# Kernel tuning notes

Hardware: AMD Instinct MI355X
Metric: run time of the kernel (lower is better)

The kernel has to match this reference:

```python
import jax, jax.numpy as jnp
import numpy as np

INF_SUB_NUM = -9000000000000000.0
LN_EPS = 1e-5


def _layernorm(x, gamma, beta):
    mu = jnp.mean(x, axis=-1, keepdims=True)
    var = jnp.mean(jnp.square(x - mu), axis=-1, keepdims=True)
    return gamma * (x - mu) * jax.lax.rsqrt(var + LN_EPS) + beta


def setup_inputs() -> dict:
    key = jax.random.key(0)
    kh, ke, kt, kw1, kw2 = jax.random.split(key, 5)
    B, N, E, D = 8, 4096, 2048, 256
    stdv = 1.0 / np.sqrt(D)
    return {
        "hidden": jax.random.normal(kh, (B, N, D), dtype=jnp.float32),
        "ht": jax.random.randint(kt, (B, E, N), 0, 2, dtype=jnp.int32),
        "edge_emb": jax.random.normal(ke, (B, E, D), dtype=jnp.float32),
        "wnk": jax.random.uniform(kw1, (D, D), jnp.float32, -stdv, stdv),
        "wek": jax.random.uniform(kw2, (D, D), jnp.float32, -stdv, stdv),
        "ln_gamma": jnp.ones((D,), jnp.float32),
        "ln_beta": jnp.zeros((D,), jnp.float32),
    }


def reference(hidden, ht, edge_emb, wnk, wek, ln_gamma, ln_beta):
    # hidden: [B,N,D]; ht: [B,E,N] incidence; edge_emb: [B,E,D]
    D = hidden.shape[-1]
    scale = 1.0 / jnp.sqrt(jnp.float32(D))

    edge_emb = _layernorm(edge_emb, ln_gamma, ln_beta)          # [B,E,D]
    node_k = hidden @ wnk                                        # [B,N,D]

    # Stage 1: edges attend over their incident nodes (softmax over N, dim=2)
    edge_scores = jnp.einsum('bed,bnd->ben', edge_emb, node_k) * scale
    edge_scores = jnp.where(ht > 0, edge_scores, INF_SUB_NUM)
    attn_edge = jax.nn.softmax(edge_scores, axis=2)              # [B,E,N]
    edge_h = jnp.einsum('ben,bnd->bed', attn_edge, hidden) + edge_emb

    # Stage 2: nodes gather from edges; softmax over N (dim=1), as in source
    edge_k = edge_h @ wek                                        # [B,E,D]
    node_scores = jnp.einsum('bnd,bed->bne', node_k, edge_k) * scale
    node_scores = jnp.where(jnp.transpose(ht, (0, 2, 1)) > 0, node_scores, INF_SUB_NUM)
    attn_node = jax.nn.softmax(node_scores, axis=1)              # [B,N,E]
    node_hidden = jnp.einsum('bne,bed->bnd', attn_node, edge_h)  # [B,N,D]
    return node_hidden
```

## Files before the change

kernel.cpp:

```cpp
#include <hip/hip_runtime.h>
#include <hip/hip_bf16.h>
#include <stdint.h>


#define B_ 8
#define N_ 4096
#define E_ 2048
#define D_ 256
#define INF_SUB (-9.0e15f)

typedef short bf16x8 __attribute__((ext_vector_type(8)));
typedef float f32x4 __attribute__((ext_vector_type(4)));
typedef unsigned short us8 __attribute__((ext_vector_type(8)));

#define AS1 __attribute__((address_space(1)))
#define AS3 __attribute__((address_space(3)))

__device__ __forceinline__ unsigned short f2bf(float f) {
    union { float f; unsigned int u; } v; v.f = f;
    unsigned int r = v.u + 0x7fffu + ((v.u >> 16) & 1u);
    return (unsigned short)(r >> 16);
}
__device__ __forceinline__ float bf2f(unsigned short h) {
    union { unsigned int u; float f; } v; v.u = ((unsigned int)h) << 16;
    return v.f;
}
__device__ __forceinline__ float waveReduceSum(float v) {
#pragma unroll
    for (int o = 32; o > 0; o >>= 1) v += __shfl_xor(v, o, 64);
    return v;
}

__global__ __launch_bounds__(256) void ln_kernel(const float* __restrict__ x,
                                                 const float* __restrict__ gamma,
                                                 const float* __restrict__ beta,
                                                 unsigned short* __restrict__ yb) {
    __shared__ float red[8];
    const int row = blockIdx.x;
    const int t = threadIdx.x;
    const int lane = t & 63, wid = t >> 6;
    const float v = x[(size_t)row * D_ + t];
    float s = waveReduceSum(v);
    if (lane == 0) red[wid] = s;
    __syncthreads();
    const float mu = (red[0] + red[1] + red[2] + red[3]) * (1.0f / D_);
    const float d = v - mu;
    float s2 = waveReduceSum(d * d);
    if (lane == 0) red[4 + wid] = s2;
    __syncthreads();
    const float var = (red[4] + red[5] + red[6] + red[7]) * (1.0f / D_);
    yb[(size_t)row * D_ + t] = f2bf(gamma[t] * d * rsqrtf(var + 1e-5f) + beta[t]);
}

__global__ __launch_bounds__(256) void pack_mask(const int* __restrict__ ht,
                                                 uint32_t* __restrict__ bits) {
    __shared__ __align__(8) unsigned char nib[256];
    const int row = blockIdx.x;
    const int t = threadIdx.x;
    const int* hrow = ht + (size_t)row * N_;
    uint32_t* brow = bits + (size_t)row * (N_ / 32);
#pragma unroll
    for (int it = 0; it < 4; ++it) {
        const int4 v = *(const int4*)&hrow[it * 1024 + t * 4];
        unsigned char n = (unsigned char)((v.x > 0) | ((v.y > 0) << 1) |
                                          ((v.z > 0) << 2) | ((v.w > 0) << 3));
        nib[t] = n;
        __syncthreads();
        if (t < 32) {
            uint64_t x = *(const uint64_t*)&nib[t * 8];
            x = (x | (x >> 4)) & 0x00FF00FF00FF00FFull;
            x = (x | (x >> 8)) & 0x0000FFFF0000FFFFull;
            brow[it * 32 + t] = (uint32_t)(x | (x >> 16));
        }
        __syncthreads();
    }
}

__global__ __launch_bounds__(256) void prep_hidden(const float* __restrict__ in,
                                                   unsigned short* __restrict__ hb,
                                                   unsigned short* __restrict__ hT) {
    __shared__ unsigned short tile[64][65];
    const int b = blockIdx.z;
    in += (size_t)b * N_ * D_;
    hb += (size_t)b * N_ * D_;
    hT += (size_t)b * D_ * N_;
    const int n0 = blockIdx.y * 64, d0 = blockIdx.x * 64;
    const int t = threadIdx.x;
    const int tr = t >> 4, tc = (t & 15) * 4;
#pragma unroll
    for (int q = 0; q < 4; ++q) {
        const int rr = q * 16 + tr;
        const float4 f = *(const float4*)&in[(size_t)(n0 + rr) * D_ + d0 + tc];
        unsigned short h0 = f2bf(f.x), h1 = f2bf(f.y), h2 = f2bf(f.z), h3 = f2bf(f.w);
        *(ushort4*)&hb[(size_t)(n0 + rr) * D_ + d0 + tc] = make_ushort4(h0, h1, h2, h3);
        tile[rr][tc + 0] = h0; tile[rr][tc + 1] = h1;
        tile[rr][tc + 2] = h2; tile[rr][tc + 3] = h3;
    }
    __syncthreads();
#pragma unroll
    for (int q = 0; q < 4; ++q) {
        const int cc = q * 16 + tr;
        ushort4 o = make_ushort4(tile[tc + 0][cc], tile[tc + 1][cc],
                                 tile[tc + 2][cc], tile[tc + 3][cc]);
        *(ushort4*)&hT[(size_t)(d0 + cc) * N_ + n0 + tc] = o;
    }
}

__global__ __launch_bounds__(256) void cast_wT(const float* __restrict__ w,
                                               unsigned short* __restrict__ wT) {
    const int gid = blockIdx.x * 256 + threadIdx.x;
    const int i = gid >> 8, j = gid & 255;
    wT[j * D_ + i] = f2bf(w[i * D_ + j]);
}

__global__ __launch_bounds__(256) void reduce_pv(const float* __restrict__ slab,
                                                 const unsigned short* __restrict__ eln,
                                                 const float* __restrict__ rsum,
                                                 unsigned short* __restrict__ eh,
                                                 float* __restrict__ ehT) {
    __shared__ float tile[64][65];
    const int b = blockIdx.z;
    const float* s0 = slab + (size_t)(b * 2) * E_ * D_;
    const float* s1 = slab + (size_t)(b * 2 + 1) * E_ * D_;
    const int e0 = blockIdx.y * 64, d0 = blockIdx.x * 64;
    const int t = threadIdx.x;
    const int tr = t >> 4, tc = (t & 15) * 4;
#pragma unroll
    for (int q = 0; q < 4; ++q) {
        const int rr = q * 16 + tr;
        const int row = e0 + rr;
        const float4 v0 = *(const float4*)&s0[(size_t)row * D_ + d0 + tc];
        const float4 v1 = *(const float4*)&s1[(size_t)row * D_ + d0 + tc];
        const float inv = 1.0f / rsum[(size_t)b * E_ + row];
        const ushort4 el = *(const ushort4*)&eln[(size_t)b * E_ * D_ + (size_t)row * D_ + d0 + tc];
        const float x0 = (v0.x + v1.x) * inv + bf2f(el.x);
        const float x1 = (v0.y + v1.y) * inv + bf2f(el.y);
        const float x2 = (v0.z + v1.z) * inv + bf2f(el.z);
        const float x3 = (v0.w + v1.w) * inv + bf2f(el.w);
        *(ushort4*)&eh[(size_t)b * E_ * D_ + (size_t)row * D_ + d0 + tc] =
            make_ushort4(f2bf(x0), f2bf(x1), f2bf(x2), f2bf(x3));
        tile[rr][tc + 0] = x0; tile[rr][tc + 1] = x1;
        tile[rr][tc + 2] = x2; tile[rr][tc + 3] = x3;
    }
    __syncthreads();
#pragma unroll
    for (int q = 0; q < 4; ++q) {
        const int cc = q * 16 + tr;
        float4 o = make_float4(tile[tc + 0][cc], tile[tc + 1][cc],
                               tile[tc + 2][cc], tile[tc + 3][cc]);
        *(float4*)&ehT[(size_t)b * D_ * E_ + (size_t)(d0 + cc) * E_ + e0 + tc] = o;
    }
}

__global__ __launch_bounds__(256) void scale_ehT(const float* __restrict__ ehT,
                                                 const float* __restrict__ lsum,
                                                 unsigned short* __restrict__ ehs) {
    const size_t base = ((size_t)blockIdx.x * 256 + threadIdx.x) * 8;
    const int b = (int)(base / ((size_t)D_ * E_));
    const int e = (int)(base % E_);
    const float4 f0 = *(const float4*)&ehT[base];
    const float4 f1 = *(const float4*)&ehT[base + 4];
    const float4 l0 = *(const float4*)&lsum[(size_t)b * E_ + e];
    const float4 l1 = *(const float4*)&lsum[(size_t)b * E_ + e + 4];
    us8 o;
    o[0] = f2bf(f0.x / l0.x); o[1] = f2bf(f0.y / l0.y);
    o[2] = f2bf(f0.z / l0.z); o[3] = f2bf(f0.w / l0.w);
    o[4] = f2bf(f1.x / l1.x); o[5] = f2bf(f1.y / l1.y);
    o[6] = f2bf(f1.z / l1.z); o[7] = f2bf(f1.w / l1.w);
    *(us8*)&ehs[base] = o;
}

#define M_BF16 0
#define M_MASK 1
#define M_F32 2

template <int MODE, int MASKOR, int RSUM, int SPLIT, int CSUM, int SWZ>
__global__ __launch_bounds__(256) void mfma_gemm_nt(
        const short* __restrict__ A, const short* __restrict__ Bm,
        void* __restrict__ Cv, const uint32_t* __restrict__ bits,
        float* __restrict__ sums,
        int K, int ldc, size_t sA, size_t sB, size_t sC, float scale) {
    __shared__ __align__(16) short ls[(MODE == M_F32) ? 16384 : 16896];
    __shared__ uint32_t mwords[MASKOR ? 512 : 4];
    short* lsA = ls;
    short* lsB = ls + 8192;
    int bx = blockIdx.x, by = blockIdx.y, bz = blockIdx.z;
    if (SWZ) {
        const int gx = gridDim.x, gy = gridDim.y;
        int lin = bx + gx * (by + gy * bz);
        const int nwg = gx * gy * (int)gridDim.z;
        lin = (lin & 7) * (nwg >> 3) + (lin >> 3);
        bx = lin % gx;
        const int t2 = lin / gx;
        by = t2 % gy;
        bz = t2 / gy;
    }
    const int zb = bz;
    const int b = SPLIT ? (zb >> 1) : zb;
    A += (size_t)b * sA;
    Bm += (size_t)b * sB;
    const int m0 = by * 128, n0 = bx * 128;
    const int tid = threadIdx.x, wid = tid >> 6, lane = tid & 63;
    const int l15 = lane & 15, kg = lane >> 4;
    const int wr = wid >> 1, wc = wid & 1;

    if (MASKOR) {
        const uint32_t* bb = bits + (size_t)b * E_ * (N_ / 32);
#pragma unroll
        for (int q = 0; q < 2; ++q) {
            const int idx = q * 256 + tid;
            mwords[idx] = (MASKOR == 1)
                ? bb[(size_t)(m0 + (idx >> 2)) * (N_ / 32) + (n0 >> 5) + (idx & 3)]
                : bb[(size_t)(n0 + (idx >> 2)) * (N_ / 32) + (m0 >> 5) + (idx & 3)];
        }
    }

    int raoff[4], rota[4], rboff[4], rotb[4];
#pragma unroll
    for (int i = 0; i < 4; ++i) {
        const int ra = wr * 64 + i * 16 + l15;
        raoff[i] = ra * 64; rota[i] = kg + (ra >> 1);
        const int rb = wc * 64 + i * 16 + l15;
        rboff[i] = rb * 64; rotb[i] = kg + (rb >> 1);
    }
    const f32x4 zero = {0.f, 0.f, 0.f, 0.f};
    f32x4 acc[4][4];
#pragma unroll
    for (int i = 0; i < 4; ++i)
#pragma unroll
        for (int j = 0; j < 4; ++j) acc[i][j] = zero;

    const int kt0 = SPLIT ? (zb & 1) * (K >> 1) : 0;
    const int ktE = SPLIT ? kt0 + (K >> 1) : K;
    for (int kt = kt0; kt < ktE; kt += 64) {
        __syncthreads();
#pragma unroll
        for (int q = 0; q < 4; ++q) {
            const int c = q * 256 + tid;
            const int r = c >> 3;
            const int kc = ((c & 7) - (r >> 1)) & 7;
            const short* ga = A + (size_t)(m0 + r) * K + kt + kc * 8;
            __builtin_amdgcn_global_load_lds((const AS1 void*)ga,
                (AS3 void*)(lsA + (q * 256 + wid * 64) * 8), 16, 0, 0);
            const short* gb = Bm + (size_t)(n0 + r) * K + kt + kc * 8;
            __builtin_amdgcn_global_load_lds((const AS1 void*)gb,
                (AS3 void*)(lsB + (q * 256 + wid * 64) * 8), 16, 0, 0);
        }
        __syncthreads();
#pragma unroll
        for (int s = 0; s < 2; ++s) {
            bf16x8 fa[4], fb[4];
#pragma unroll
            for (int i = 0; i < 4; ++i)
                fa[i] = *(const bf16x8*)(lsA + raoff[i] + (((s * 4 + rota[i]) & 7) << 3));
#pragma unroll
            for (int j = 0; j < 4; ++j)
                fb[j] = *(const bf16x8*)(lsB + rboff[j] + (((s * 4 + rotb[j]) & 7) << 3));
#pragma unroll
            for (int i = 0; i < 4; ++i)
#pragma unroll
                for (int j = 0; j < 4; ++j)
                    acc[i][j] = __builtin_amdgcn_mfma_f32_16x16x32_bf16(fa[i], fb[j], acc[i][j], 0, 0, 0);
        }
    }

    __syncthreads();

    if (MODE == M_F32) {
        float* C = (float*)Cv + (SPLIT ? (size_t)zb * sC : (size_t)b * sC);
        float* lsF = (float*)ls;
#pragma unroll
        for (int h = 0; h < 4; ++h) {
            if (wr == (h >> 1)) {
#pragma unroll
                for (int ii = 0; ii < 2; ++ii) {
                    const int i = (h & 1) * 2 + ii;
#pragma unroll
                    for (int j = 0; j < 4; ++j)
#pragma unroll
                        for (int r = 0; r < 4; ++r) {
                            const int rl = ii * 16 + kg * 4 + r;
                            const int cl = wc * 64 + j * 16 + l15;
                            lsF[rl * 128 + cl] = acc[i][j][r];
                        }
                }
            }
            __syncthreads();
#pragma unroll
            for (int si = 0; si < 4; ++si) {
                const int row = (tid >> 5) + si * 8;
                const int colb = (tid & 31) * 4;
                float4 v = *(float4*)&lsF[row * 128 + colb];
                *(float4*)&C[(size_t)(m0 + h * 32 + row) * ldc + n0 + colb] = v;
            }
            __syncthreads();
        }
    } else {
        unsigned short* C = (unsigned short*)Cv + (size_t)b * sC;
        float evsum[4] = {0.f, 0.f, 0.f, 0.f};
#pragma unroll
        for (int i = 0; i < 4; ++i) {
#pragma unroll
            for (int r = 0; r < 4; ++r) {
                const int rowfull = wr * 64 + i * 16 + kg * 4 + r;
                uint64_t mwr = 0;
                if (MODE == M_MASK && MASKOR == 1)
                    mwr = *(const uint64_t*)&mwords[rowfull * 4 + wc * 2];
                float rs = 0.f;
#pragma unroll
                for (int j = 0; j < 4; ++j) {
                    const int cl = wc * 64 + j * 16 + l15;
                    float v = acc[i][j][r];
                    if (MODE == M_MASK) {
                        v *= scale;
                        uint32_t bit;
                        if (MASKOR == 1) {
                            bit = (uint32_t)(mwr >> (j * 16 + l15)) & 1u;
                        } else {
                            const uint64_t mwc = *(const uint64_t*)&mwords[cl * 4 + wr * 2];
                            bit = (uint32_t)(mwc >> (i * 16 + kg * 4 + r)) & 1u;
                        }
                        v = bit ? __expf(v) : 0.f;
                        if (CSUM) evsum[j] += v;
                        if (RSUM) rs += v;
                    }
                    ls[rowfull * 132 + cl] = (short)f2bf(v);
                }
                if (RSUM) {
                    rs += __shfl_xor(rs, 1, 64);
                    rs += __shfl_xor(rs, 2, 64);
                    rs += __shfl_xor(rs, 4, 64);
                    rs += __shfl_xor(rs, 8, 64);
                    if (l15 == 0)
                        atomicAdd(&sums[(size_t)b * E_ + m0 + rowfull], rs);
                }
            }
        }
        __syncthreads();
#pragma unroll
        for (int si = 0; si < 8; ++si) {
            const int row = (tid >> 4) + si * 16;
            const int col = (tid & 15) * 8;
            us8 val = *(us8*)&ls[row * 132 + col];
            *(us8*)&C[(size_t)(m0 + row) * ldc + n0 + col] = val;
        }
        if (CSUM) {
#pragma unroll
            for (int j = 0; j < 4; ++j) {
                float cs = evsum[j];
                cs += __shfl_xor(cs, 16, 64);
                cs += __shfl_xor(cs, 32, 64);
                if (kg == 0)
                    atomicAdd(&sums[(size_t)b * E_ + n0 + wc * 64 + j * 16 + l15], cs);
            }
        }
    }
}

extern "C" void kernel_launch(void* const* d_in, const int* in_sizes, int n_in,
                              void* d_out, int out_size, void* d_ws, size_t ws_size,
                              hipStream_t stream) {
    const float* hidden = (const float*)d_in[0];
    const int* ht = (const int*)d_in[1];
    const float* edge_emb = (const float*)d_in[2];
    const float* wnk = (const float*)d_in[3];
    const float* wek = (const float*)d_in[4];
    const float* gamma = (const float*)d_in[5];
    const float* beta = (const float*)d_in[6];
    float* out = (float*)d_out;
    (void)in_sizes; (void)n_in; (void)out_size; (void)ws_size;

    char* w = (char*)d_ws;
    unsigned short* SP = (unsigned short*)w;         w += (size_t)B_ * E_ * N_ * 2;
    unsigned short* hidden_bf = (unsigned short*)w;  w += (size_t)B_ * N_ * D_ * 2;
    unsigned short* hiddenT_bf = (unsigned short*)w; w += (size_t)B_ * D_ * N_ * 2;
    unsigned short* node_k_bf = (unsigned short*)w;  w += (size_t)B_ * N_ * D_ * 2;
    unsigned short* eln_bf = (unsigned short*)w;     w += (size_t)B_ * E_ * D_ * 2;
    unsigned short* edge_h_bf = (unsigned short*)w;  w += (size_t)B_ * E_ * D_ * 2;
    float* ehT_f32 = (float*)w;                      w += (size_t)B_ * D_ * E_ * 4;
    unsigned short* ehsT_bf = (unsigned short*)w;    w += (size_t)B_ * D_ * E_ * 2;
    unsigned short* edge_k_bf = (unsigned short*)w;  w += (size_t)B_ * E_ * D_ * 2;
    float* slabs = (float*)w;                        w += (size_t)B_ * 2 * E_ * D_ * 4;
    uint32_t* bits = (uint32_t*)w;                   w += (size_t)B_ * E_ * (N_ / 32) * 4;
    float* rsum = (float*)w;                         w += (size_t)B_ * E_ * 4;
    float* lsum = (float*)w;                         w += (size_t)B_ * E_ * 4;
    unsigned short* wnkT = (unsigned short*)w;       w += (size_t)D_ * D_ * 2;
    unsigned short* wekT = (unsigned short*)w;       w += (size_t)D_ * D_ * 2;

    const float scale = 0.0625f;

    prep_hidden<<<dim3(D_ / 64, N_ / 64, B_), 256, 0, stream>>>(hidden, hidden_bf, hiddenT_bf);
    cast_wT<<<D_ * D_ / 256, 256, 0, stream>>>(wnk, wnkT);
    cast_wT<<<D_ * D_ / 256, 256, 0, stream>>>(wek, wekT);
    ln_kernel<<<B_ * E_, 256, 0, stream>>>(edge_emb, gamma, beta, eln_bf);
    pack_mask<<<B_ * E_, 256, 0, stream>>>(ht, bits);
    hipMemsetAsync(rsum, 0, (size_t)B_ * E_ * 8, stream);

    mfma_gemm_nt<M_BF16, 0, 0, 0, 0, 0><<<dim3(D_ / 128, (B_ * N_) / 128, 1), 256, 0, stream>>>(
        (const short*)hidden_bf, (const short*)wnkT, node_k_bf, nullptr, nullptr,
        D_, D_, 0, 0, 0, 1.f);
    mfma_gemm_nt<M_MASK, 1, 1, 0, 0, 1><<<dim3(N_ / 128, E_ / 128, B_), 256, 0, stream>>>(
        (const short*)eln_bf, (const short*)node_k_bf, SP, bits, rsum,
        D_, N_, (size_t)E_ * D_, (size_t)N_ * D_, (size_t)E_ * N_, scale);
    mfma_gemm_nt<M_F32, 0, 0, 1, 0, 1><<<dim3(D_ / 128, E_ / 128, B_ * 2), 256, 0, stream>>>(
        (const short*)SP, (const short*)hiddenT_bf, slabs, nullptr, nullptr,
        N_, D_, (size_t)E_ * N_, (size_t)D_ * N_, (size_t)E_ * D_, 1.f);
    reduce_pv<<<dim3(D_ / 64, E_ / 64, B_), 256, 0, stream>>>(
        slabs, eln_bf, rsum, edge_h_bf, ehT_f32);
    mfma_gemm_nt<M_BF16, 0, 0, 0, 0, 0><<<dim3(D_ / 128, (B_ * E_) / 128, 1), 256, 0, stream>>>(
        (const short*)edge_h_bf, (const short*)wekT, edge_k_bf, nullptr, nullptr,
        D_, D_, 0, 0, 0, 1.f);
    mfma_gemm_nt<M_MASK, 2, 0, 0, 1, 1><<<dim3(E_ / 128, N_ / 128, B_), 256, 0, stream>>>(
        (const short*)node_k_bf, (const short*)edge_k_bf, SP, bits, lsum,
        D_, E_, (size_t)N_ * D_, (size_t)E_ * D_, (size_t)N_ * E_, scale);
    scale_ehT<<<(B_ * D_ * E_) / (256 * 8), 256, 0, stream>>>(ehT_f32, lsum, ehsT_bf);
    mfma_gemm_nt<M_F32, 0, 0, 0, 0, 1><<<dim3(D_ / 128, N_ / 128, B_), 256, 0, stream>>>(
        (const short*)SP, (const short*)ehsT_bf, out, nullptr, nullptr,
        E_, D_, (size_t)N_ * E_, (size_t)D_ * E_, (size_t)N_ * D_, 1.f);
}
```

Measured before the change: 790.3 us.

## Add 64x256 wide GEMM for PV products, drop split-K slabs

Replaces the two attention-times-value GEMMs (K=4096 split-K into two fp32 slabs, and K=2048 output GEMM) with a new kernel using 64x256 output tiles spanning the full D dimension. The big probability matrix SP is then read once per row block instead of twice (once per 128-column D half), and the split-K slab reduction in reduce_pv goes away. The XCD-style block swizzle is removed from the generic GEMM and applied only in the wide kernel. The trade-off is less parallelism without split-K (256 blocks for stage 1) and more registers per thread (32 accumulators of 4 floats), which may lower occupancy.

```diff
diff --git a/kernel.cpp b/kernel.cpp
--- a/kernel.cpp
+++ b/kernel.cpp
@@ -120,8 +120,7 @@
                                                  float* __restrict__ ehT) {
     __shared__ float tile[64][65];
     const int b = blockIdx.z;
-    const float* s0 = slab + (size_t)(b * 2) * E_ * D_;
-    const float* s1 = slab + (size_t)(b * 2 + 1) * E_ * D_;
+    const float* s0 = slab + (size_t)b * E_ * D_;
     const int e0 = blockIdx.y * 64, d0 = blockIdx.x * 64;
     const int t = threadIdx.x;
     const int tr = t >> 4, tc = (t & 15) * 4;
@@ -130,13 +129,12 @@
         const int rr = q * 16 + tr;
         const int row = e0 + rr;
         const float4 v0 = *(const float4*)&s0[(size_t)row * D_ + d0 + tc];
-        const float4 v1 = *(const float4*)&s1[(size_t)row * D_ + d0 + tc];
         const float inv = 1.0f / rsum[(size_t)b * E_ + row];
         const ushort4 el = *(const ushort4*)&eln[(size_t)b * E_ * D_ + (size_t)row * D_ + d0 + tc];
-        const float x0 = (v0.x + v1.x) * inv + bf2f(el.x);
-        const float x1 = (v0.y + v1.y) * inv + bf2f(el.y);
-        const float x2 = (v0.z + v1.z) * inv + bf2f(el.z);
-        const float x3 = (v0.w + v1.w) * inv + bf2f(el.w);
+        const float x0 = v0.x * inv + bf2f(el.x);
+        const float x1 = v0.y * inv + bf2f(el.y);
+        const float x2 = v0.z * inv + bf2f(el.z);
+        const float x3 = v0.w * inv + bf2f(el.w);
         *(ushort4*)&eh[(size_t)b * E_ * D_ + (size_t)row * D_ + d0 + tc] =
             make_ushort4(f2bf(x0), f2bf(x1), f2bf(x2), f2bf(x3));
         tile[rr][tc + 0] = x0; tile[rr][tc + 1] = x1;
@@ -174,7 +172,7 @@
 #define M_MASK 1
 #define M_F32 2
 
-template <int MODE, int MASKOR, int RSUM, int SPLIT, int CSUM, int SWZ>
+template <int MODE, int MASKOR, int RSUM, int SPLIT, int CSUM>
 __global__ __launch_bounds__(256) void mfma_gemm_nt(
         const short* __restrict__ A, const short* __restrict__ Bm,
         void* __restrict__ Cv, const uint32_t* __restrict__ bits,
@@ -184,22 +182,11 @@
     __shared__ uint32_t mwords[MASKOR ? 512 : 4];
     short* lsA = ls;
     short* lsB = ls + 8192;
-    int bx = blockIdx.x, by = blockIdx.y, bz = blockIdx.z;
-    if (SWZ) {
-        const int gx = gridDim.x, gy = gridDim.y;
-        int lin = bx + gx * (by + gy * bz);
-        const int nwg = gx * gy * (int)gridDim.z;
-        lin = (lin & 7) * (nwg >> 3) + (lin >> 3);
-        bx = lin % gx;
-        const int t2 = lin / gx;
-        by = t2 % gy;
-        bz = t2 / gy;
-    }
-    const int zb = bz;
+    const int zb = blockIdx.z;
     const int b = SPLIT ? (zb >> 1) : zb;
     A += (size_t)b * sA;
     Bm += (size_t)b * sB;
-    const int m0 = by * 128, n0 = bx * 128;
+    const int m0 = blockIdx.y * 128, n0 = blockIdx.x * 128;
     const int tid = threadIdx.x, wid = tid >> 6, lane = tid & 63;
     const int l15 = lane & 15, kg = lane >> 4;
     const int wr = wid >> 1, wc = wid & 1;
@@ -357,6 +344,110 @@
     }
 }
 
+__global__ __launch_bounds__(256) void mfma_gemm_wide(
+        const short* __restrict__ A, const short* __restrict__ Bm,
+        float* __restrict__ C,
+        int K, size_t sA, size_t sB, size_t sC) {
+    __shared__ __align__(16) short ls[20480];
+    short* lsA = ls;
+    short* lsB = ls + 4096;
+    const int gx = gridDim.x;
+    int lin = blockIdx.x + gx * blockIdx.y;
+    const int nwg = gx * (int)gridDim.y;
+    lin = (lin & 7) * (nwg >> 3) + (lin >> 3);
+    const int bm = lin % gx, bb = lin / gx;
+    A += (size_t)bb * sA;
+    Bm += (size_t)bb * sB;
+    C += (size_t)bb * sC;
+    const int m0 = bm * 64;
+    const int tid = threadIdx.x, wid = tid >> 6, lane = tid & 63;
+    const int l15 = lane & 15, kg = lane >> 4;
+    const int wr = wid >> 1, wc = wid & 1;
+
+    int raoff[2], rota[2], rboff[8], rotb[8];
+#pragma unroll
+    for (int i = 0; i < 2; ++i) {
+        const int ra = wr * 32 + i * 16 + l15;
+        raoff[i] = ra * 64; rota[i] = kg + (ra >> 1);
+    }
+#pragma unroll
+    for (int j = 0; j < 8; ++j) {
+        const int rb = wc * 128 + j * 16 + l15;
+        rboff[j] = rb * 64; rotb[j] = kg + (rb >> 1);
+    }
+    const f32x4 zero = {0.f, 0.f, 0.f, 0.f};
+    f32x4 acc[2][8];
+#pragma unroll
+    for (int i = 0; i < 2; ++i)
+#pragma unroll
+        for (int j = 0; j < 8; ++j) acc[i][j] = zero;
+
+    for (int kt = 0; kt < K; kt += 64) {
+        __syncthreads();
+#pragma unroll
+        for (int q = 0; q < 2; ++q) {
+            const int c = q * 256 + tid;
+            const int r = c >> 3;
+            const int kc = ((c & 7) - (r >> 1)) & 7;
+            const short* ga = A + (size_t)(m0 + r) * K + kt + kc * 8;
+            __builtin_amdgcn_global_load_lds((const AS1 void*)ga,
+                (AS3 void*)(lsA + (q * 256 + wid * 64) * 8), 16, 0, 0);
+        }
+#pragma unroll
+        for (int q = 0; q < 8; ++q) {
+            const int c = q * 256 + tid;
+            const int r = c >> 3;
+            const int kc = ((c & 7) - (r >> 1)) & 7;
+            const short* gb = Bm + (size_t)r * K + kt + kc * 8;
+            __builtin_amdgcn_global_load_lds((const AS1 void*)gb,
+                (AS3 void*)(lsB + (q * 256 + wid * 64) * 8), 16, 0, 0);
+        }
+        __syncthreads();
+#pragma unroll
+        for (int s = 0; s < 2; ++s) {
+            bf16x8 fa[2], fb[8];
+#pragma unroll
+            for (int i = 0; i < 2; ++i)
+                fa[i] = *(const bf16x8*)(lsA + raoff[i] + (((s * 4 + rota[i]) & 7) << 3));
+#pragma unroll
+            for (int j = 0; j < 8; ++j)
+                fb[j] = *(const bf16x8*)(lsB + rboff[j] + (((s * 4 + rotb[j]) & 7) << 3));
+#pragma unroll
+            for (int i = 0; i < 2; ++i)
+#pragma unroll
+                for (int j = 0; j < 8; ++j)
+                    acc[i][j] = __builtin_amdgcn_mfma_f32_16x16x32_bf16(fa[i], fb[j], acc[i][j], 0, 0, 0);
+        }
+    }
+
+    __syncthreads();
+    float* lsF = (float*)ls;
+#pragma unroll
+    for (int h = 0; h < 2; ++h) {
+        if (wr == h) {
+#pragma unroll
+            for (int i = 0; i < 2; ++i)
+#pragma unroll
+                for (int j = 0; j < 8; ++j)
+#pragma unroll
+                    for (int r = 0; r < 4; ++r) {
+                        const int row = i * 16 + kg * 4 + r;
+                        const int col = wc * 128 + j * 16 + l15;
+                        lsF[row * 256 + col] = acc[i][j][r];
+                    }
+        }
+        __syncthreads();
+#pragma unroll
+        for (int k = 0; k < 8; ++k) {
+            const int c = k * 256 + tid;
+            const int row = c >> 6;
+            const int c4 = (c & 63) * 4;
+            *(float4*)&C[(size_t)(m0 + h * 32 + row) * D_ + c4] = *(float4*)&lsF[row * 256 + c4];
+        }
+        __syncthreads();
+    }
+}
+
 extern "C" void kernel_launch(void* const* d_in, const int* in_sizes, int n_in,
                               void* d_out, int out_size, void* d_ws, size_t ws_size,
                               hipStream_t stream) {
@@ -380,7 +471,7 @@
     float* ehT_f32 = (float*)w;                      w += (size_t)B_ * D_ * E_ * 4;
     unsigned short* ehsT_bf = (unsigned short*)w;    w += (size_t)B_ * D_ * E_ * 2;
     unsigned short* edge_k_bf = (unsigned short*)w;  w += (size_t)B_ * E_ * D_ * 2;
-    float* slabs = (float*)w;                        w += (size_t)B_ * 2 * E_ * D_ * 4;
+    float* edge_sum = (float*)w;                     w += (size_t)B_ * E_ * D_ * 4;
     uint32_t* bits = (uint32_t*)w;                   w += (size_t)B_ * E_ * (N_ / 32) * 4;
     float* rsum = (float*)w;                         w += (size_t)B_ * E_ * 4;
     float* lsum = (float*)w;                         w += (size_t)B_ * E_ * 4;
@@ -396,25 +487,25 @@
     pack_mask<<<B_ * E_, 256, 0, stream>>>(ht, bits);
     hipMemsetAsync(rsum, 0, (size_t)B_ * E_ * 8, stream);
 
-    mfma_gemm_nt<M_BF16, 0, 0, 0, 0, 0><<<dim3(D_ / 128, (B_ * N_) / 128, 1), 256, 0, stream>>>(
+    mfma_gemm_nt<M_BF16, 0, 0, 0, 0><<<dim3(D_ / 128, (B_ * N_) / 128, 1), 256, 0, stream>>>(
         (const short*)hidden_bf, (const short*)wnkT, node_k_bf, nullptr, nullptr,
         D_, D_, 0, 0, 0, 1.f);
-    mfma_gemm_nt<M_MASK, 1, 1, 0, 0, 1><<<dim3(N_ / 128, E_ / 128, B_), 256, 0, stream>>>(
+    mfma_gemm_nt<M_MASK, 1, 1, 0, 0><<<dim3(N_ / 128, E_ / 128, B_), 256, 0, stream>>>(
         (const short*)eln_bf, (const short*)node_k_bf, SP, bits, rsum,
         D_, N_, (size_t)E_ * D_, (size_t)N_ * D_, (size_t)E_ * N_, scale);
-    mfma_gemm_nt<M_F32, 0, 0, 1, 0, 1><<<dim3(D_ / 128, E_ / 128, B_ * 2), 256, 0, stream>>>(
-        (const short*)SP, (const short*)hiddenT_bf, slabs, nullptr, nullptr,
-        N_, D_, (size_t)E_ * N_, (size_t)D_ * N_, (size_t)E_ * D_, 1.f);
+    mfma_gemm_wide<<<dim3(E_ / 64, B_), 256, 0, stream>>>(
+        (const short*)SP, (const short*)hiddenT_bf, edge_sum,
+        N_, (size_t)E_ * N_, (size_t)D_ * N_, (size_t)E_ * D_);
     reduce_pv<<<dim3(D_ / 64, E_ / 64, B_), 256, 0, stream>>>(
-        slabs, eln_bf, rsum, edge_h_bf, ehT_f32);
-    mfma_gemm_nt<M_BF16, 0, 0, 0, 0, 0><<<dim3(D_ / 128, (B_ * E_) / 128, 1), 256, 0, stream>>>(
+        edge_sum, eln_bf, rsum, edge_h_bf, ehT_f32);
+    mfma_gemm_nt<M_BF16, 0, 0, 0, 0><<<dim3(D_ / 128, (B_ * E_) / 128, 1), 256, 0, stream>>>(
         (const short*)edge_h_bf, (const short*)wekT, edge_k_bf, nullptr, nullptr,
         D_, D_, 0, 0, 0, 1.f);
-    mfma_gemm_nt<M_MASK, 2, 0, 0, 1, 1><<<dim3(E_ / 128, N_ / 128, B_), 256, 0, stream>>>(
+    mfma_gemm_nt<M_MASK, 2, 0, 0, 1><<<dim3(E_ / 128, N_ / 128, B_), 256, 0, stream>>>(
         (const short*)node_k_bf, (const short*)edge_k_bf, SP, bits, lsum,
         D_, E_, (size_t)N_ * D_, (size_t)E_ * D_, (size_t)N_ * E_, scale);
     scale_ehT<<<(B_ * D_ * E_) / (256 * 8), 256, 0, stream>>>(ehT_f32, lsum, ehsT_bf);
-    mfma_gemm_nt<M_F32, 0, 0, 0, 0, 1><<<dim3(D_ / 128, N_ / 128, B_), 256, 0, stream>>>(
-        (const short*)SP, (const short*)ehsT_bf, out, nullptr, nullptr,
-        E_, D_, (size_t)N_ * E_, (size_t)D_ * E_, (size_t)N_ * D_, 1.f);
-}
+    mfma_gemm_wide<<<dim3(N_ / 64, B_), 256, 0, stream>>>(
+        (const short*)SP, (const short*)ehsT_bf, out,
+        E_, (size_t)N_ * E_, (size_t)D_ * E_, (size_t)N_ * D_);
+}
```

Result: no change. 802.9 us (+1.6%).

## Fuse masked score, exp and PV GEMMs into flash-style attention kernels

Applied to the files above, without the earlier changes.

Replaces the separate score-GEMM, materialized bf16 probability matrix SP, and PV GEMM with fused kernels that compute masked exp scores per 64-column tile, stage them through LDS, and immediately accumulate P·V in registers. This removes the large B×E×N intermediate round-trip through global memory, the split-K slabs, the reduce kernel, and atomics. For stage 2 the column sums are computed in a separate score-only pass (MODE 0), and the scores are recomputed in the final fused pass, so that GEMM is done twice. It also uses large LDS and one block per CU, which may limit occupancy.

```diff
diff --git a/kernel.cpp b/kernel.cpp
--- a/kernel.cpp
+++ b/kernel.cpp
@@ -7,7 +7,6 @@
 #define N_ 4096
 #define E_ 2048
 #define D_ 256
-#define INF_SUB (-9.0e15f)
 
 typedef short bf16x8 __attribute__((ext_vector_type(8)));
 typedef float f32x4 __attribute__((ext_vector_type(4)));
@@ -113,45 +112,6 @@
     wT[j * D_ + i] = f2bf(w[i * D_ + j]);
 }
 
-__global__ __launch_bounds__(256) void reduce_pv(const float* __restrict__ slab,
-                                                 const unsigned short* __restrict__ eln,
-                                                 const float* __restrict__ rsum,
-                                                 unsigned short* __restrict__ eh,
-                                                 float* __restrict__ ehT) {
-    __shared__ float tile[64][65];
-    const int b = blockIdx.z;
-    const float* s0 = slab + (size_t)(b * 2) * E_ * D_;
-    const float* s1 = slab + (size_t)(b * 2 + 1) * E_ * D_;
-    const int e0 = blockIdx.y * 64, d0 = blockIdx.x * 64;
-    const int t = threadIdx.x;
-    const int tr = t >> 4, tc = (t & 15) * 4;
-#pragma unroll
-    for (int q = 0; q < 4; ++q) {
-        const int rr = q * 16 + tr;
-        const int row = e0 + rr;
-        const float4 v0 = *(const float4*)&s0[(size_t)row * D_ + d0 + tc];
-        const float4 v1 = *(const float4*)&s1[(size_t)row * D_ + d0 + tc];
-        const float inv = 1.0f / rsum[(size_t)b * E_ + row];
-        const ushort4 el = *(const ushort4*)&eln[(size_t)b * E_ * D_ + (size_t)row * D_ + d0 + tc];
-        const float x0 = (v0.x + v1.x) * inv + bf2f(el.x);
-        const float x1 = (v0.y + v1.y) * inv + bf2f(el.y);
-        const float x2 = (v0.z + v1.z) * inv + bf2f(el.z);
-        const float x3 = (v0.w + v1.w) * inv + bf2f(el.w);
-        *(ushort4*)&eh[(size_t)b * E_ * D_ + (size_t)row * D_ + d0 + tc] =
-            make_ushort4(f2bf(x0), f2bf(x1), f2bf(x2), f2bf(x3));
-        tile[rr][tc + 0] = x0; tile[rr][tc + 1] = x1;
-        tile[rr][tc + 2] = x2; tile[rr][tc + 3] = x3;
-    }
-    __syncthreads();
-#pragma unroll
-    for (int q = 0; q < 4; ++q) {
-        const int cc = q * 16 + tr;
-        float4 o = make_float4(tile[tc + 0][cc], tile[tc + 1][cc],
-                               tile[tc + 2][cc], tile[tc + 3][cc]);
-        *(float4*)&ehT[(size_t)b * D_ * E_ + (size_t)(d0 + cc) * E_ + e0 + tc] = o;
-    }
-}
-
 __global__ __launch_bounds__(256) void scale_ehT(const float* __restrict__ ehT,
                                                  const float* __restrict__ lsum,
                                                  unsigned short* __restrict__ ehs) {
@@ -170,50 +130,16 @@
     *(us8*)&ehs[base] = o;
 }
 
-#define M_BF16 0
-#define M_MASK 1
-#define M_F32 2
-
-template <int MODE, int MASKOR, int RSUM, int SPLIT, int CSUM, int SWZ>
-__global__ __launch_bounds__(256) void mfma_gemm_nt(
-        const short* __restrict__ A, const short* __restrict__ Bm,
-        void* __restrict__ Cv, const uint32_t* __restrict__ bits,
-        float* __restrict__ sums,
-        int K, int ldc, size_t sA, size_t sB, size_t sC, float scale) {
-    __shared__ __align__(16) short ls[(MODE == M_F32) ? 16384 : 16896];
-    __shared__ uint32_t mwords[MASKOR ? 512 : 4];
+__global__ __launch_bounds__(256) void gemm_bf16(const short* __restrict__ A,
+                                                 const short* __restrict__ Bm,
+                                                 unsigned short* __restrict__ C) {
+    __shared__ __align__(16) short ls[16896];
     short* lsA = ls;
     short* lsB = ls + 8192;
-    int bx = blockIdx.x, by = blockIdx.y, bz = blockIdx.z;
-    if (SWZ) {
-        const int gx = gridDim.x, gy = gridDim.y;
-        int lin = bx + gx * (by + gy * bz);
-        const int nwg = gx * gy * (int)gridDim.z;
-        lin = (lin & 7) * (nwg >> 3) + (lin >> 3);
-        bx = lin % gx;
-        const int t2 = lin / gx;
-        by = t2 % gy;
-        bz = t2 / gy;
-    }
-    const int zb = bz;
-    const int b = SPLIT ? (zb >> 1) : zb;
-    A += (size_t)b * sA;
-    Bm += (size_t)b * sB;
-    const int m0 = by * 128, n0 = bx * 128;
+    const int m0 = blockIdx.y * 128, n0 = blockIdx.x * 128;
     const int tid = threadIdx.x, wid = tid >> 6, lane = tid & 63;
     const int l15 = lane & 15, kg = lane >> 4;
     const int wr = wid >> 1, wc = wid & 1;
-
-    if (MASKOR) {
-        const uint32_t* bb = bits + (size_t)b * E_ * (N_ / 32);
-#pragma unroll
-        for (int q = 0; q < 2; ++q) {
-            const int idx = q * 256 + tid;
-            mwords[idx] = (MASKOR == 1)
-                ? bb[(size_t)(m0 + (idx >> 2)) * (N_ / 32) + (n0 >> 5) + (idx & 3)]
-                : bb[(size_t)(n0 + (idx >> 2)) * (N_ / 32) + (m0 >> 5) + (idx & 3)];
-        }
-    }
 
     int raoff[4], rota[4], rboff[4], rotb[4];
 #pragma unroll
@@ -230,19 +156,17 @@
 #pragma unroll
         for (int j = 0; j < 4; ++j) acc[i][j] = zero;
 
-    const int kt0 = SPLIT ? (zb & 1) * (K >> 1) : 0;
-    const int ktE = SPLIT ? kt0 + (K >> 1) : K;
-    for (int kt = kt0; kt < ktE; kt += 64) {
+    for (int kt = 0; kt < 256; kt += 64) {
         __syncthreads();
 #pragma unroll
         for (int q = 0; q < 4; ++q) {
             const int c = q * 256 + tid;
             const int r = c >> 3;
             const int kc = ((c & 7) - (r >> 1)) & 7;
-            const short* ga = A + (size_t)(m0 + r) * K + kt + kc * 8;
+            const short* ga = A + (size_t)(m0 + r) * 256 + kt + kc * 8;
             __builtin_amdgcn_global_load_lds((const AS1 void*)ga,
                 (AS3 void*)(lsA + (q * 256 + wid * 64) * 8), 16, 0, 0);
-            const short* gb = Bm + (size_t)(n0 + r) * K + kt + kc * 8;
+            const short* gb = Bm + (size_t)(n0 + r) * 256 + kt + kc * 8;
             __builtin_amdgcn_global_load_lds((const AS1 void*)gb,
                 (AS3 void*)(lsB + (q * 256 + wid * 64) * 8), 16, 0, 0);
         }
@@ -263,96 +187,268 @@
                     acc[i][j] = __builtin_amdgcn_mfma_f32_16x16x32_bf16(fa[i], fb[j], acc[i][j], 0, 0, 0);
         }
     }
-
     __syncthreads();
-
-    if (MODE == M_F32) {
-        float* C = (float*)Cv + (SPLIT ? (size_t)zb * sC : (size_t)b * sC);
+#pragma unroll
+    for (int i = 0; i < 4; ++i)
+#pragma unroll
+        for (int r = 0; r < 4; ++r) {
+            const int rowfull = wr * 64 + i * 16 + kg * 4 + r;
+#pragma unroll
+            for (int j = 0; j < 4; ++j) {
+                const int cl = wc * 64 + j * 16 + l15;
+                ls[rowfull * 132 + cl] = (short)f2bf(acc[i][j][r]);
+            }
+        }
+    __syncthreads();
+#pragma unroll
+    for (int si = 0; si < 8; ++si) {
+        const int row = (tid >> 4) + si * 16;
+        const int col = (tid & 15) * 8;
+        us8 val = *(us8*)&ls[row * 132 + col];
+        *(us8*)&C[(size_t)(m0 + row) * D_ + n0 + col] = val;
+    }
+}
+
+template <int MODE>
+__global__ __launch_bounds__(256, 1) void fused_attn(
+        const short* __restrict__ A, const short* __restrict__ B1,
+        const short* __restrict__ B2, const uint32_t* __restrict__ bits,
+        const unsigned short* __restrict__ eln,
+        void* __restrict__ out1, float* __restrict__ out2,
+        int KN, float scale) {
+    __shared__ __align__(16) short ls[(MODE == 0) ? 33024 : 69888];
+    const int b = blockIdx.x;
+    const int m0 = blockIdx.y * 64;
+    const int MA = (MODE == 2) ? N_ : E_;
+    const short* Ab = A + (size_t)b * MA * D_;
+    const short* B1b = B1 + (size_t)b * KN * D_;
+    const short* B2b = (MODE != 0) ? (B2 + (size_t)b * D_ * KN) : nullptr;
+    const uint32_t* bb = bits + (size_t)b * E_ * (N_ / 32);
+
+    const int tid = threadIdx.x, wid = tid >> 6, lane = tid & 63;
+    const int l15 = lane & 15, kg = lane >> 4;
+    const int wv = wid >> 1, ww = wid & 1;
+
+    bf16x8 fa[2][8];
+#pragma unroll
+    for (int mf = 0; mf < 2; ++mf) {
+        const size_t ar = (size_t)(m0 + wv * 32 + mf * 16 + l15) * D_;
+#pragma unroll
+        for (int kf = 0; kf < 8; ++kf)
+            fa[mf][kf] = *(const bf16x8*)(Ab + ar + (kf * 4 + kg) * 8);
+    }
+
+    const f32x4 zero = {0.f, 0.f, 0.f, 0.f};
+    f32x4 acco[2][8];
+    if (MODE != 0) {
+#pragma unroll
+        for (int mf = 0; mf < 2; ++mf)
+#pragma unroll
+            for (int jf = 0; jf < 8; ++jf) acco[mf][jf] = zero;
+    }
+    float rs[2][4] = {{0.f, 0.f, 0.f, 0.f}, {0.f, 0.f, 0.f, 0.f}};
+
+    short* Pp = ls + 65536;
+    const int NT = KN / 64;
+
+#define STAGE_T(db, tt) do {                                                   \
+        const int kt_ = (tt) * 64;                                             \
+        short* b1d_ = ls + (db) * 16384;                                       \
+        _Pragma("unroll")                                                      \
+        for (int q = 0; q < 8; ++q) {                                          \
+            const int c_ = q * 256 + tid;                                      \
+            const int r_ = c_ >> 5;                                            \
+            const int ck_ = (c_ & 31) ^ (r_ & 31);                             \
+            __builtin_amdgcn_global_load_lds(                                  \
+                (const AS1 void*)(B1b + (size_t)(kt_ + r_) * D_ + ck_ * 8),    \
+                (AS3 void*)(b1d_ + (q * 256 + wid * 64) * 8), 16, 0, 0);       \
+        }                                                                      \
+        if (MODE != 0) {                                                       \
+            short* b2d_ = ls + 32768 + (db) * 16384;                           \
+            _Pragma("unroll")                                                  \
+            for (int q = 0; q < 8; ++q) {                                      \
+                const int c_ = q * 256 + tid;                                  \
+                const int r_ = c_ >> 3;                                        \
+                const int ck_ = (c_ & 7) ^ ((r_ >> 1) & 7);                    \
+                __builtin_amdgcn_global_load_lds(                              \
+                    (const AS1 void*)(B2b + (size_t)r_ * KN + kt_ + ck_ * 8),  \
+                    (AS3 void*)(b2d_ + (q * 256 + wid * 64) * 8), 16, 0, 0);   \
+            }                                                                  \
+        }                                                                      \
+    } while (0)
+
+    STAGE_T(0, 0);
+    __syncthreads();
+
+    int cur = 0;
+    for (int t = 0; t < NT; ++t) {
+        if (t + 1 < NT) STAGE_T(cur ^ 1, t + 1);
+        const short* b1c = ls + cur * 16384;
+        f32x4 accs[2][2];
+        accs[0][0] = zero; accs[0][1] = zero; accs[1][0] = zero; accs[1][1] = zero;
+        const int rb0 = ww * 32 + l15, rb1 = ww * 32 + 16 + l15;
+        const int x0 = kg ^ (rb0 & 31), x1 = kg ^ (rb1 & 31);
+#pragma unroll
+        for (int kf = 0; kf < 8; ++kf) {
+            const bf16x8 fb0 = *(const bf16x8*)(b1c + rb0 * 256 + ((kf * 4) ^ x0) * 8);
+            const bf16x8 fb1 = *(const bf16x8*)(b1c + rb1 * 256 + ((kf * 4) ^ x1) * 8);
+            accs[0][0] = __builtin_amdgcn_mfma_f32_16x16x32_bf16(fa[0][kf], fb0, accs[0][0], 0, 0, 0);
+            accs[1][0] = __builtin_amdgcn_mfma_f32_16x16x32_bf16(fa[1][kf], fb0, accs[1][0], 0, 0, 0);
+            accs[0][1] = __builtin_amdgcn_mfma_f32_16x16x32_bf16(fa[0][kf], fb1, accs[0][1], 0, 0, 0);
+            accs[1][1] = __builtin_amdgcn_mfma_f32_16x16x32_bf16(fa[1][kf], fb1, accs[1][1], 0, 0, 0);
+        }
+        const int kt0 = t * 64;
+        uint64_t mw[2][4];
+        uint32_t cw[2];
+        if (MODE <= 1) {
+#pragma unroll
+            for (int mf = 0; mf < 2; ++mf)
+#pragma unroll
+                for (int r = 0; r < 4; ++r) {
+                    const int row = m0 + wv * 32 + mf * 16 + kg * 4 + r;
+                    mw[mf][r] = *(const uint64_t*)&bb[(size_t)row * (N_ / 32) + (kt0 >> 5)];
+                }
+        } else {
+#pragma unroll
+            for (int jf = 0; jf < 2; ++jf) {
+                const int col = kt0 + ww * 32 + jf * 16 + l15;
+                cw[jf] = bb[(size_t)col * (N_ / 32) + ((m0 + wv * 32) >> 5)];
+            }
+        }
+#pragma unroll
+        for (int mf = 0; mf < 2; ++mf)
+#pragma unroll
+            for (int jf = 0; jf < 2; ++jf)
+#pragma unroll
+                for (int r = 0; r < 4; ++r) {
+                    float v = accs[mf][jf][r] * scale;
+                    uint32_t bit;
+                    if (MODE <= 1)
+                        bit = (uint32_t)(mw[mf][r] >> (ww * 32 + jf * 16 + l15)) & 1u;
+                    else
+                        bit = (cw[jf] >> (mf * 16 + kg * 4 + r)) & 1u;
+                    v = bit ? __expf(v) : 0.f;
+                    if (MODE <= 1) rs[mf][r] += v;
+                    if (MODE != 0) {
+                        const int prow = wv * 32 + mf * 16 + kg * 4 + r;
+                        const int pcol = ww * 32 + jf * 16 + l15;
+                        Pp[prow * 64 + (((pcol >> 3) ^ ((prow >> 1) & 7)) * 8) + (pcol & 7)] =
+                            (short)f2bf(v);
+                    }
+                }
+        if (MODE != 0) {
+            __syncthreads();
+            const short* b2c = ls + 32768 + cur * 16384;
+            const int pr0 = wv * 32 + l15, pr1 = wv * 32 + 16 + l15;
+            const int px0 = kg ^ ((pr0 >> 1) & 7), px1 = kg ^ ((pr1 >> 1) & 7);
+#pragma unroll
+            for (int kf2 = 0; kf2 < 2; ++kf2) {
+                const bf16x8 pa0 = *(const bf16x8*)(Pp + pr0 * 64 + ((kf2 * 4) ^ px0) * 8);
+                const bf16x8 pa1 = *(const bf16x8*)(Pp + pr1 * 64 + ((kf2 * 4) ^ px1) * 8);
+#pragma unroll
+                for (int jf = 0; jf < 8; ++jf) {
+                    const int rh = ww * 128 + jf * 16 + l15;
+                    const bf16x8 fbh = *(const bf16x8*)(b2c + rh * 64 +
+                        (((kf2 * 4 + kg) ^ ((rh >> 1) & 7))) * 8);
+                    acco[0][jf] = __builtin_amdgcn_mfma_f32_16x16x32_bf16(pa0, fbh, acco[0][jf], 0, 0, 0);
+                    acco[1][jf] = __builtin_amdgcn_mfma_f32_16x16x32_bf16(pa1, fbh, acco[1][jf], 0, 0, 0);
+                }
+            }
+        }
+        __syncthreads();
+        cur ^= 1;
+    }
+#undef STAGE_T
+
+    if (MODE == 0) {
+        float* rsx = (float*)(ls + 32768);
+#pragma unroll
+        for (int mf = 0; mf < 2; ++mf)
+#pragma unroll
+            for (int r = 0; r < 4; ++r) {
+                float s = rs[mf][r];
+                s += __shfl_xor(s, 1, 64); s += __shfl_xor(s, 2, 64);
+                s += __shfl_xor(s, 4, 64); s += __shfl_xor(s, 8, 64);
+                if (l15 == 0) rsx[ww * 64 + wv * 32 + mf * 16 + kg * 4 + r] = s;
+            }
+        __syncthreads();
+        if (tid < 64)
+            ((float*)out1)[(size_t)b * E_ + m0 + tid] = rsx[tid] + rsx[64 + tid];
+    } else if (MODE == 1) {
+        float* rsx = (float*)(ls + 69632);
+#pragma unroll
+        for (int mf = 0; mf < 2; ++mf)
+#pragma unroll
+            for (int r = 0; r < 4; ++r) {
+                float s = rs[mf][r];
+                s += __shfl_xor(s, 1, 64); s += __shfl_xor(s, 2, 64);
+                s += __shfl_xor(s, 4, 64); s += __shfl_xor(s, 8, 64);
+                if (l15 == 0) rsx[ww * 64 + wv * 32 + mf * 16 + kg * 4 + r] = s;
+            }
+        __syncthreads();
         float* lsF = (float*)ls;
 #pragma unroll
-        for (int h = 0; h < 4; ++h) {
-            if (wr == (h >> 1)) {
-#pragma unroll
-                for (int ii = 0; ii < 2; ++ii) {
-                    const int i = (h & 1) * 2 + ii;
-#pragma unroll
-                    for (int j = 0; j < 4; ++j)
-#pragma unroll
-                        for (int r = 0; r < 4; ++r) {
-                            const int rl = ii * 16 + kg * 4 + r;
-                            const int cl = wc * 64 + j * 16 + l15;
-                            lsF[rl * 128 + cl] = acc[i][j][r];
-                        }
-                }
-            }
-            __syncthreads();
-#pragma unroll
-            for (int si = 0; si < 4; ++si) {
-                const int row = (tid >> 5) + si * 8;
-                const int colb = (tid & 31) * 4;
-                float4 v = *(float4*)&lsF[row * 128 + colb];
-                *(float4*)&C[(size_t)(m0 + h * 32 + row) * ldc + n0 + colb] = v;
-            }
-            __syncthreads();
+        for (int mf = 0; mf < 2; ++mf)
+#pragma unroll
+            for (int r = 0; r < 4; ++r) {
+                const int row = wv * 32 + mf * 16 + kg * 4 + r;
+                const float inv = 1.0f / (rsx[row] + rsx[64 + row]);
+#pragma unroll
+                for (int jf = 0; jf < 8; ++jf)
+                    lsF[row * 261 + ww * 128 + jf * 16 + l15] = acco[mf][jf][r] * inv;
+            }
+        __syncthreads();
+        unsigned short* ehb = (unsigned short*)out1 + (size_t)b * E_ * D_;
+        const unsigned short* elnb = eln + (size_t)b * E_ * D_;
+#pragma unroll
+        for (int p = 0; p < 8; ++p) {
+            const int idx = p * 2048 + tid * 8;
+            const int row = idx >> 8, col = idx & 255;
+            const us8 ev = *(const us8*)&elnb[(size_t)(m0 + row) * D_ + col];
+            us8 o;
+            float vv[8];
+#pragma unroll
+            for (int u = 0; u < 8; ++u) {
+                vv[u] = lsF[row * 261 + col + u] + bf2f(ev[u]);
+                o[u] = f2bf(vv[u]);
+            }
+            *(us8*)&ehb[(size_t)(m0 + row) * D_ + col] = o;
+#pragma unroll
+            for (int u = 0; u < 8; ++u)
+                lsF[row * 261 + col + u] = vv[u];
+        }
+        __syncthreads();
+        float* ehT = out2 + (size_t)b * D_ * E_;
+#pragma unroll
+        for (int p = 0; p < 8; ++p) {
+            const int idx = p * 2048 + tid * 8;
+            const int d = idx >> 6, e8 = idx & 63;
+            float4 v0, v1;
+            v0.x = lsF[(e8 + 0) * 261 + d]; v0.y = lsF[(e8 + 1) * 261 + d];
+            v0.z = lsF[(e8 + 2) * 261 + d]; v0.w = lsF[(e8 + 3) * 261 + d];
+            v1.x = lsF[(e8 + 4) * 261 + d]; v1.y = lsF[(e8 + 5) * 261 + d];
+            v1.z = lsF[(e8 + 6) * 261 + d]; v1.w = lsF[(e8 + 7) * 261 + d];
+            *(float4*)&ehT[(size_t)d * E_ + m0 + e8] = v0;
+            *(float4*)&ehT[(size_t)d * E_ + m0 + e8 + 4] = v1;
         }
     } else {
-        unsigned short* C = (unsigned short*)Cv + (size_t)b * sC;
-        float evsum[4] = {0.f, 0.f, 0.f, 0.f};
-#pragma unroll
-        for (int i = 0; i < 4; ++i) {
+        float* lsF = (float*)ls;
+#pragma unroll
+        for (int mf = 0; mf < 2; ++mf)
 #pragma unroll
             for (int r = 0; r < 4; ++r) {
-                const int rowfull = wr * 64 + i * 16 + kg * 4 + r;
-                uint64_t mwr = 0;
-                if (MODE == M_MASK && MASKOR == 1)
-                    mwr = *(const uint64_t*)&mwords[rowfull * 4 + wc * 2];
-                float rs = 0.f;
-#pragma unroll
-                for (int j = 0; j < 4; ++j) {
-                    const int cl = wc * 64 + j * 16 + l15;
-                    float v = acc[i][j][r];
-                    if (MODE == M_MASK) {
-                        v *= scale;
-                        uint32_t bit;
-                        if (MASKOR == 1) {
-                            bit = (uint32_t)(mwr >> (j * 16 + l15)) & 1u;
-                        } else {
-                            const uint64_t mwc = *(const uint64_t*)&mwords[cl * 4 + wr * 2];
-                            bit = (uint32_t)(mwc >> (i * 16 + kg * 4 + r)) & 1u;
-                        }
-                        v = bit ? __expf(v) : 0.f;
-                        if (CSUM) evsum[j] += v;
-                        if (RSUM) rs += v;
-                    }
-                    ls[rowfull * 132 + cl] = (short)f2bf(v);
-                }
-                if (RSUM) {
-                    rs += __shfl_xor(rs, 1, 64);
-                    rs += __shfl_xor(rs, 2, 64);
-                    rs += __shfl_xor(rs, 4, 64);
-                    rs += __shfl_xor(rs, 8, 64);
-                    if (l15 == 0)
-                        atomicAdd(&sums[(size_t)b * E_ + m0 + rowfull], rs);
-                }
-            }
-        }
-        __syncthreads();
-#pragma unroll
-        for (int si = 0; si < 8; ++si) {
-            const int row = (tid >> 4) + si * 16;
-            const int col = (tid & 15) * 8;
-            us8 val = *(us8*)&ls[row * 132 + col];
-            *(us8*)&C[(size_t)(m0 + row) * ldc + n0 + col] = val;
-        }
-        if (CSUM) {
-#pragma unroll
-            for (int j = 0; j < 4; ++j) {
-                float cs = evsum[j];
-                cs += __shfl_xor(cs, 16, 64);
-                cs += __shfl_xor(cs, 32, 64);
-                if (kg == 0)
-                    atomicAdd(&sums[(size_t)b * E_ + n0 + wc * 64 + j * 16 + l15], cs);
-            }
+                const int row = wv * 32 + mf * 16 + kg * 4 + r;
+#pragma unroll
+                for (int jf = 0; jf < 8; ++jf)
+                    lsF[row * 256 + ww * 128 + jf * 16 + l15] = acco[mf][jf][r];
+            }
+        __syncthreads();
+        float* ob = (float*)out1 + (size_t)b * N_ * D_;
+#pragma unroll
+        for (int p = 0; p < 16; ++p) {
+            const int lin = p * 256 + tid;
+            const int row = lin >> 6, c4 = (lin & 63) * 4;
+            *(float4*)&ob[(size_t)(m0 + row) * D_ + c4] = *(const float4*)&lsF[row * 256 + c4];
         }
     }
 }
@@ -371,7 +467,6 @@
     (void)in_sizes; (void)n_in; (void)out_size; (void)ws_size;
 
     char* w = (char*)d_ws;
-    unsigned short* SP = (unsigned short*)w;         w += (size_t)B_ * E_ * N_ * 2;
     unsigned short* hidden_bf = (unsigned short*)w;  w += (size_t)B_ * N_ * D_ * 2;
     unsigned short* hiddenT_bf = (unsigned short*)w; w += (size_t)B_ * D_ * N_ * 2;
     unsigned short* node_k_bf = (unsigned short*)w;  w += (size_t)B_ * N_ * D_ * 2;
@@ -380,9 +475,7 @@
     float* ehT_f32 = (float*)w;                      w += (size_t)B_ * D_ * E_ * 4;
     unsigned short* ehsT_bf = (unsigned short*)w;    w += (size_t)B_ * D_ * E_ * 2;
     unsigned short* edge_k_bf = (unsigned short*)w;  w += (size_t)B_ * E_ * D_ * 2;
-    float* slabs = (float*)w;                        w += (size_t)B_ * 2 * E_ * D_ * 4;
     uint32_t* bits = (uint32_t*)w;                   w += (size_t)B_ * E_ * (N_ / 32) * 4;
-    float* rsum = (float*)w;                         w += (size_t)B_ * E_ * 4;
     float* lsum = (float*)w;                         w += (size_t)B_ * E_ * 4;
     unsigned short* wnkT = (unsigned short*)w;       w += (size_t)D_ * D_ * 2;
     unsigned short* wekT = (unsigned short*)w;       w += (size_t)D_ * D_ * 2;
@@ -394,27 +487,19 @@
     cast_wT<<<D_ * D_ / 256, 256, 0, stream>>>(wek, wekT);
     ln_kernel<<<B_ * E_, 256, 0, stream>>>(edge_emb, gamma, beta, eln_bf);
     pack_mask<<<B_ * E_, 256, 0, stream>>>(ht, bits);
-    hipMemsetAsync(rsum, 0, (size_t)B_ * E_ * 8, stream);
-
-    mfma_gemm_nt<M_BF16, 0, 0, 0, 0, 0><<<dim3(D_ / 128, (B_ * N_) / 128, 1), 256, 0, stream>>>(
-        (const short*)hidden_bf, (const short*)wnkT, node_k_bf, nullptr, nullptr,
-        D_, D_, 0, 0, 0, 1.f);
-    mfma_gemm_nt<M_MASK, 1, 1, 0, 0, 1><<<dim3(N_ / 128, E_ / 128, B_), 256, 0, stream>>>(
-        (const short*)eln_bf, (const short*)node_k_bf, SP, bits, rsum,
-        D_, N_, (size_t)E_ * D_, (size_t)N_ * D_, (size_t)E_ * N_, scale);
-    mfma_gemm_nt<M_F32, 0, 0, 1, 0, 1><<<dim3(D_ / 128, E_ / 128, B_ * 2), 256, 0, stream>>>(
-        (const short*)SP, (const short*)hiddenT_bf, slabs, nullptr, nullptr,
-        N_, D_, (size_t)E_ * N_, (size_t)D_ * N_, (size_t)E_ * D_, 1.f);
-    reduce_pv<<<dim3(D_ / 64, E_ / 64, B_), 256, 0, stream>>>(
-        slabs, eln_bf, rsum, edge_h_bf, ehT_f32);
-    mfma_gemm_nt<M_BF16, 0, 0, 0, 0, 0><<<dim3(D_ / 128, (B_ * E_) / 128, 1), 256, 0, stream>>>(
-        (const short*)edge_h_bf, (const short*)wekT, edge_k_bf, nullptr, nullptr,
-        D_, D_, 0, 0, 0, 1.f);
-    mfma_gemm_nt<M_MASK, 2, 0, 0, 1, 1><<<dim3(E_ / 128, N_ / 128, B_), 256, 0, stream>>>(
-        (const short*)node_k_bf, (const short*)edge_k_bf, SP, bits, lsum,
-        D_, E_, (size_t)N_ * D_, (size_t)E_ * D_, (size_t)N_ * E_, scale);
+
+    gemm_bf16<<<dim3(D_ / 128, (B_ * N_) / 128), 256, 0, stream>>>(
+        (const short*)hidden_bf, (const short*)wnkT, node_k_bf);
+    fused_attn<1><<<dim3(8, E_ / 64), 256, 0, stream>>>(
+        (const short*)eln_bf, (const short*)node_k_bf, (const short*)hiddenT_bf,
+        bits, eln_bf, edge_h_bf, ehT_f32, N_, scale);
+    gemm_bf16<<<dim3(D_ / 128, (B_ * E_) / 128), 256, 0, stream>>>(
+        (const short*)edge_h_bf, (const short*)wekT, edge_k_bf);
+    fused_attn<0><<<dim3(8, E_ / 64), 256, 0, stream>>>(
+        (const short*)edge_k_bf, (const short*)node_k_bf, nullptr,
+        bits, nullptr, lsum, nullptr, N_, scale);
     scale_ehT<<<(B_ * D_ * E_) / (256 * 8), 256, 0, stream>>>(ehT_f32, lsum, ehsT_bf);
-    mfma_gemm_nt<M_F32, 0, 0, 0, 0, 1><<<dim3(D_ / 128, N_ / 128, B_), 256, 0, stream>>>(
-        (const short*)SP, (const short*)ehsT_bf, out, nullptr, nullptr,
-        E_, D_, (size_t)N_ * E_, (size_t)D_ * E_, (size_t)N_ * D_, 1.f);
-}
+    fused_attn<2><<<dim3(8, N_ / 64), 256, 0, stream>>>(
+        (const short*)node_k_bf, (const short*)edge_k_bf, (const short*)ehsT_bf,
+        bits, nullptr, out, nullptr, E_, scale);
+}
```

New measurement: 894.6 us. 13.2% more time.
